# Kernel tuning notes

Hardware: AMD Instinct MI355X
Metric: run time of the kernel (lower is better)

The kernel has to match this reference:

```python
import jax, jax.numpy as jnp
import numpy as np

D_MODEL, D_INNER, D_STATE, D_CONV, DT_RANK = 4, 8, 16, 4, 1


def _build_perms(N, H, W):
    # center-out 2D spatial order
    yy, xx = np.meshgrid(np.arange(H), np.arange(W), indexing='ij')
    cy, cx = H // 2, W // 2
    d2 = (yy - cy) ** 2 + (xx - cx) ** 2
    sp = np.argsort(d2.reshape(-1), kind='stable')          # (H*W,)
    HW = H * W
    # scanA: for each frame t, full center-out spatial sweep
    scanA = (np.arange(N)[:, None] * HW + sp[None, :]).reshape(-1)
    # scanB: for each spatial pos (in center-out order), zig-zag over frames
    fwd = np.arange(N)
    bwd = fwd[::-1]
    tids = np.where((np.arange(HW) % 2 == 0)[:, None], fwd[None, :], bwd[None, :])  # (HW, N)
    scanB = (tids * HW + sp[:, None]).reshape(-1)
    perms = np.stack([scanA, scanB, scanA[::-1], scanB[::-1]], axis=0)  # (4, L)
    return jnp.asarray(perms)


def _dwconv1d(x_bcl, w, b, pad, groups):
    # x: (B, C, L), w: (C, 1, K) depthwise
    y = jax.lax.conv_general_dilated(x_bcl, w, (1,), [pad],
                                     feature_group_count=groups,
                                     dimension_numbers=('NCH', 'OIH', 'NCH'))
    return y + b[None, :, None]


def _forward(x, dwconv_w, dwconv_b, in_proj_w, conv1d_w, conv1d_b,
             x_proj_w, dt_proj_w, dt_proj_b, A_log, Dp, out_proj_w, ln_g, ln_b):
    B, N, H, W = x.shape
    L = N * H * W
    perms = _build_perms(N, H, W)                 # (4, L) int, static
    xf = x.reshape(B, L)
    seqs = xf[:, perms]                            # (B, 4, L) gather along 4 scans
    seqs = _dwconv1d(seqs, dwconv_w, dwconv_b, (1, 1), 4)
    u = jax.nn.silu(seqs.transpose(0, 2, 1))       # (B, L, 4)
    # ---- Mamba(d_model=4) ----
    xz = jnp.einsum('bld,ed->ble', u, in_proj_w)   # (B, L, 2*d_inner)
    xm, z = xz[..., :D_INNER], xz[..., D_INNER:]
    xc = _dwconv1d(xm.transpose(0, 2, 1), conv1d_w, conv1d_b, (D_CONV - 1, 0), D_INNER)
    xm = jax.nn.silu(xc.transpose(0, 2, 1))        # (B, L, 8) causal conv + SiLU
    x_dbl = jnp.einsum('bld,ed->ble', xm, x_proj_w)  # (B, L, dt_rank+2*d_state)
    dt = x_dbl[..., :DT_RANK]
    Bm = x_dbl[..., DT_RANK:DT_RANK + D_STATE]     # (B, L, 16)
    Cm = x_dbl[..., DT_RANK + D_STATE:]            # (B, L, 16)
    dt = jax.nn.softplus(jnp.einsum('blr,dr->bld', dt, dt_proj_w) + dt_proj_b)  # (B, L, 8)
    A = -jnp.exp(A_log)                            # (8, 16)
    dA = jnp.exp(dt[..., None] * A)                # (B, L, 8, 16)
    dBx = dt[..., None] * Bm[:, :, None, :] * xm[..., None]  # (B, L, 8, 16)

    def step(h, inp):
        dA_t, dBx_t, C_t = inp
        h = dA_t * h + dBx_t                       # (B, 8, 16)
        return h, jnp.einsum('bds,bs->bd', h, C_t)

    h0 = jnp.zeros((B, D_INNER, D_STATE), x.dtype)
    _, ys = jax.lax.scan(step, h0, (dA.transpose(1, 0, 2, 3),
                                    dBx.transpose(1, 0, 2, 3),
                                    Cm.transpose(1, 0, 2)))
    y = ys.transpose(1, 0, 2) + xm * Dp            # (B, L, 8)
    y = y * jax.nn.silu(z)
    out = jnp.einsum('bld,ed->ble', y, out_proj_w)  # (B, L, 4)
    # ---- LayerNorm(4) ----
    mu = out.mean(-1, keepdims=True)
    var = ((out - mu) ** 2).mean(-1, keepdims=True)
    out = (out - mu) * jax.lax.rsqrt(var + 1e-5) * ln_g + ln_b
    # rec[:, inv[i]] = out[:, :, i]  <=>  rec_i = out[:, perms[i], i]
    rec = jnp.take_along_axis(out, perms.T[None], axis=1)  # (B, L, 4)
    return rec.mean(-1).reshape(B, N, H, W)


def setup_inputs() -> dict:
    key = jax.random.key(0)
    ks = jax.random.split(key, 12)
    s = 0.1
    x = jax.random.normal(ks[0], (4, 6, 128, 128), jnp.float32)
    return {
        'x': x,
        'dwconv_w': jax.random.normal(ks[1], (4, 1, 3), jnp.float32) * s,
        'dwconv_b': jnp.zeros((4,), jnp.float32),
        'in_proj_w': jax.random.normal(ks[2], (2 * D_INNER, D_MODEL), jnp.float32) * s,
        'conv1d_w': jax.random.normal(ks[3], (D_INNER, 1, D_CONV), jnp.float32) * s,
        'conv1d_b': jnp.zeros((D_INNER,), jnp.float32),
        'x_proj_w': jax.random.normal(ks[4], (DT_RANK + 2 * D_STATE, D_INNER), jnp.float32) * s,
        'dt_proj_w': jax.random.normal(ks[5], (D_INNER, DT_RANK), jnp.float32) * s,
        'dt_proj_b': jnp.full((D_INNER,), -2.0, jnp.float32),
        'A_log': jnp.log(jnp.tile(jnp.arange(1, D_STATE + 1, dtype=jnp.float32), (D_INNER, 1))),
        'Dp': jnp.ones((D_INNER,), jnp.float32),
        'out_proj_w': jax.random.normal(ks[6], (D_MODEL, D_INNER), jnp.float32) * s,
        'ln_g': jnp.ones((4,), jnp.float32),
        'ln_b': jnp.zeros((4,), jnp.float32),
    }


def reference(x, dwconv_w, dwconv_b, in_proj_w, conv1d_w, conv1d_b,
              x_proj_w, dt_proj_w, dt_proj_b, A_log, Dp, out_proj_w, ln_g, ln_b):
    return _forward(x, dwconv_w, dwconv_b, in_proj_w, conv1d_w, conv1d_b,
                    x_proj_w, dt_proj_w, dt_proj_b, A_log, Dp, out_proj_w, ln_g, ln_b)
```

## Files before the change

kernel.cpp:

```cpp
#include <hip/hip_runtime.h>
#include <math.h>

#define HWSZ  16384
#define LTOT  98304
#define NB    4
#define TCH   96
#define NCH   1024
#define GCH   64
#define NGRP  16
#define SD    100

__device__ __forceinline__ float siluf(float x){
  return x * __builtin_amdgcn_rcpf(1.f + __expf(-x));
}
__device__ __forceinline__ float softplusf(float x){
  return fmaxf(x, 0.f) + __logf(1.f + __expf(-fabsf(x)));
}

__device__ __forceinline__ float red16(float x){
  int v;
  v = __float_as_int(x);
  x += __int_as_float(__builtin_amdgcn_update_dpp(0, v, 0xB1, 0xF, 0xF, true));
  v = __float_as_int(x);
  x += __int_as_float(__builtin_amdgcn_update_dpp(0, v, 0x4E, 0xF, 0xF, true));
  v = __float_as_int(x);
  x += __int_as_float(__builtin_amdgcn_update_dpp(0, v, 0x141, 0xF, 0xF, true));
  v = __float_as_int(x);
  x += __int_as_float(__builtin_amdgcn_update_dpp(0, v, 0x140, 0xF, 0xF, true));
  return x;
}

__device__ __forceinline__ int rho0(int i, const int* __restrict__ sp){
  int n = i >> 14; int r = i & (HWSZ - 1);
  return (n << 14) + sp[r];
}
__device__ __forceinline__ int rho1(int i, const int* __restrict__ sp){
  unsigned ui = (unsigned)i;
  unsigned r = ui / 6u; unsigned n = ui - r * 6u;
  unsigned t = (r & 1u) ? (5u - n) : n;
  return (int)((t << 14) + (unsigned)sp[r]);
}

__global__ __launch_bounds__(256) void k_rank(int* __restrict__ sp){
  __shared__ int hist[8193];
  __shared__ int part[256];
  const int tid = threadIdx.x;
  for (int v = tid; v < 8193; v += 256) hist[v] = 0;
  __syncthreads();
  for (int jj = tid; jj < HWSZ; jj += 256){
    int dy = (jj >> 7) - 64, dx = (jj & 127) - 64;
    atomicAdd(&hist[dy*dy + dx*dx], 1);
  }
  __syncthreads();
  const int base = tid * 33;
  {
    int sum = 0;
    for (int m = 0; m < 33; ++m){ int v = base + m; if (v < 8193) sum += hist[v]; }
    part[tid] = sum;
  }
  __syncthreads();
  if (tid == 0){
    int run = 0;
    for (int t = 0; t < 256; ++t){ int c = part[t]; part[t] = run; run += c; }
  }
  __syncthreads();
  {
    int run = part[tid];
    for (int m = 0; m < 33; ++m){
      int v = base + m;
      if (v < 8193){ int c = hist[v]; hist[v] = run; run += c; }
    }
  }
  __syncthreads();

  const int j = blockIdx.x * 256 + tid;
  const int y = j >> 7, x = j & 127;
  const int dy = y - 64, dx = x - 64;
  const int v = dy*dy + dx*dx;
  int cnt = hist[v];
  const int r = __float2int_rd(sqrtf((float)v));
  int yp0 = 64 - r; if (yp0 < 0) yp0 = 0;
  int yp1 = 64 + r + 1; if (yp1 > y) yp1 = y;
  for (int yp = yp0; yp < yp1; ++yp){
    int dyp = yp - 64;
    int tt = v - dyp*dyp;
    int rr = __float2int_rn(sqrtf((float)tt));
    if (rr * rr == tt){
      cnt += (rr <= 64) ? 1 : 0;
      cnt += (rr >= 1 && rr <= 63) ? 1 : 0;
    }
  }
  if (x > 64) cnt += 1;
  sp[cnt] = j;
}

__global__ __launch_bounds__(128, 4)
void k_scan(const float* __restrict__ X,
            const float* __restrict__ dww, const float* __restrict__ dwb,
            const float* __restrict__ ipw,
            const float* __restrict__ c1w, const float* __restrict__ c1b,
            const float* __restrict__ xpw,
            const float* __restrict__ dtpw, const float* __restrict__ dtpb,
            const float* __restrict__ Alog,
            const int* __restrict__ sp,
            float* __restrict__ chA, float* __restrict__ chB,
            float* __restrict__ y0g, float4* __restrict__ ug4)
{
  const int c = blockIdx.x, b = blockIdx.y;
  const int c0 = c * TCH;
  const int tid = threadIdx.x;
  const float* Xb = X + (size_t)b * LTOT;

  __shared__ __align__(16) float s_pre[(TCH + 3) * 9];
  __shared__ __align__(16) float s_dt[8 * SD];
  __shared__ __align__(16) float s_dxm[8 * SD];
  __shared__ __align__(16) float s_Bv[16 * SD];
  __shared__ __align__(16) float s_Cv[16 * SD];

  if (tid < TCH + 3){
    const int m = tid;
    const int i = c0 - 3 + m;
    if (i < 0){
      #pragma unroll
      for (int d = 0; d < 8; ++d) s_pre[m*9 + d] = 0.f;
    } else {
      const int i2 = LTOT - 1 - i;
      const bool okm = (i > 0), okp = (i < LTOT - 1);
      int q[12];
      q[0]  = okm ? rho0(i - 1, sp) : 0;
      q[1]  =       rho0(i,     sp);
      q[2]  = okp ? rho0(i + 1, sp) : 0;
      q[3]  = okm ? rho1(i - 1, sp) : 0;
      q[4]  =       rho1(i,     sp);
      q[5]  = okp ? rho1(i + 1, sp) : 0;
      q[6]  = okm ? rho0(i2 + 1, sp) : 0;
      q[7]  =       rho0(i2,     sp);
      q[8]  = okp ? rho0(i2 - 1, sp) : 0;
      q[9]  = okm ? rho1(i2 + 1, sp) : 0;
      q[10] =       rho1(i2,     sp);
      q[11] = okp ? rho1(i2 - 1, sp) : 0;
      float xv[12];
      #pragma unroll
      for (int t = 0; t < 12; ++t) xv[t] = Xb[q[t]];
      if (!okm){ xv[0] = 0.f; xv[3] = 0.f; xv[6] = 0.f; xv[9]  = 0.f; }
      if (!okp){ xv[2] = 0.f; xv[5] = 0.f; xv[8] = 0.f; xv[11] = 0.f; }
      float u[4];
      #pragma unroll
      for (int k = 0; k < 4; ++k){
        float acc = dwb[k];
        acc = fmaf(dww[k*3+0], xv[k*3+0], acc);
        acc = fmaf(dww[k*3+1], xv[k*3+1], acc);
        acc = fmaf(dww[k*3+2], xv[k*3+2], acc);
        u[k] = siluf(acc);
      }
      ug4[(size_t)b * LTOT + i] = make_float4(u[0], u[1], u[2], u[3]);
      #pragma unroll
      for (int d = 0; d < 8; ++d){
        float acc =      ipw[d*4+0] * u[0];
        acc = fmaf(ipw[d*4+1], u[1], acc);
        acc = fmaf(ipw[d*4+2], u[2], acc);
        acc = fmaf(ipw[d*4+3], u[3], acc);
        s_pre[m*9 + d] = acc;
      }
    }
  }
  __syncthreads();

  if (tid < TCH){
    const int t = tid;
    float xm[8];
    #pragma unroll
    for (int d = 0; d < 8; ++d){
      float acc = c1b[d];
      #pragma unroll
      for (int tau = 0; tau < 4; ++tau)
        acc = fmaf(c1w[d*4+tau], s_pre[(t+tau)*9 + d], acc);
      xm[d] = siluf(acc);
    }
    float dtr = xpw[0] * xm[0];
    #pragma unroll
    for (int d = 1; d < 8; ++d) dtr = fmaf(xpw[d], xm[d], dtr);
    #pragma unroll
    for (int s = 0; s < 16; ++s){
      float acc = xpw[(1+s)*8] * xm[0];
      #pragma unroll
      for (int d = 1; d < 8; ++d) acc = fmaf(xpw[(1+s)*8+d], xm[d], acc);
      s_Bv[s*SD + t] = acc;
      float acc2 = xpw[(17+s)*8] * xm[0];
      #pragma unroll
      for (int d = 1; d < 8; ++d) acc2 = fmaf(xpw[(17+s)*8+d], xm[d], acc2);
      s_Cv[s*SD + t] = acc2;
    }
    #pragma unroll
    for (int d = 0; d < 8; ++d){
      float dtv = softplusf(fmaf(dtpw[d], dtr, dtpb[d]));
      s_dt[d*SD + t]  = dtv;
      s_dxm[d*SD + t] = dtv * xm[d];
    }
  }
  __syncthreads();

  {
    const int d = tid >> 4, s = tid & 15;
    const float Ads = -__expf(Alog[tid]);
    float h = 0.f, sdt = 0.f;
    const float* pdt = s_dt + d*SD;
    const float* pdx = s_dxm + d*SD;
    const float* pB  = s_Bv + s*SD;
    const float* pC  = s_Cv + s*SD;
    float* yb = y0g + ((size_t)b * NCH + c) * 768 + d * 96;
    for (int t0 = 0; t0 < TCH; t0 += 4){
      const float4 dt4 = *reinterpret_cast<const float4*>(pdt + t0);
      const float4 dx4 = *reinterpret_cast<const float4*>(pdx + t0);
      const float4 B4  = *reinterpret_cast<const float4*>(pB + t0);
      const float4 C4  = *reinterpret_cast<const float4*>(pC + t0);
      sdt += dt4.x + dt4.y + dt4.z + dt4.w;
      float y0, y1, y2, y3;
      { float dA = __expf(dt4.x*Ads); h = fmaf(dA, h, dx4.x*B4.x); y0 = h*C4.x; }
      { float dA = __expf(dt4.y*Ads); h = fmaf(dA, h, dx4.y*B4.y); y1 = h*C4.y; }
      { float dA = __expf(dt4.z*Ads); h = fmaf(dA, h, dx4.z*B4.z); y2 = h*C4.z; }
      { float dA = __expf(dt4.w*Ads); h = fmaf(dA, h, dx4.w*B4.w); y3 = h*C4.w; }
      y0 = red16(y0); y1 = red16(y1); y2 = red16(y2); y3 = red16(y3);
      if (s == 0)
        *reinterpret_cast<float4*>(yb + t0) = make_float4(y0, y1, y2, y3);
    }
    const size_t base = ((size_t)b * NCH + c) * 128 + tid;
    chA[base] = __expf(Ads * sdt);
    chB[base] = h;
  }
}

__global__ __launch_bounds__(128) void k_comb1(const float* __restrict__ chA,
                                               const float* __restrict__ chB,
                                               float* __restrict__ hpre,
                                               float* __restrict__ apre,
                                               float* __restrict__ GA,
                                               float* __restrict__ GB){
  const int j = blockIdx.x;
  const int g = j >> 2, b = j & 3;
  const int idx = threadIdx.x;
  const size_t base = ((size_t)b * NCH + (size_t)g * GCH) * 128 + idx;
  float h = 0.f, a = 1.f;
  float A_[8], B_[8];
  #pragma unroll
  for (int m = 0; m < 8; ++m){ A_[m] = chA[base + (size_t)m*128]; B_[m] = chB[base + (size_t)m*128]; }
  for (int cc = 0; cc < GCH; cc += 8){
    float A2[8], B2[8];
    if (cc + 8 < GCH){
      #pragma unroll
      for (int m = 0; m < 8; ++m){ A2[m] = chA[base + (size_t)(cc+8+m)*128]; B2[m] = chB[base + (size_t)(cc+8+m)*128]; }
    } else {
      #pragma unroll
      for (int m = 0; m < 8; ++m){ A2[m] = 0.f; B2[m] = 0.f; }
    }
    #pragma unroll
    for (int m = 0; m < 8; ++m){
      hpre[base + (size_t)(cc+m)*128] = h;
      apre[base + (size_t)(cc+m)*128] = a;
      h = fmaf(A_[m], h, B_[m]);
      a *= A_[m];
    }
    #pragma unroll
    for (int m = 0; m < 8; ++m){ A_[m] = A2[m]; B_[m] = B2[m]; }
  }
  GA[(size_t)(g*4+b)*128 + idx] = a;
  GB[(size_t)(g*4+b)*128 + idx] = h;
}

#define NBL (NB * LTOT)
__global__ __launch_bounds__(128, 4)
void k_corr(const float4* __restrict__ ug4,
            const float* __restrict__ ipw,
            const float* __restrict__ c1w, const float* __restrict__ c1b,
            const float* __restrict__ xpw,
            const float* __restrict__ dtpw, const float* __restrict__ dtpb,
            const float* __restrict__ Alog, const float* __restrict__ Dp,
            const float* __restrict__ opw,
            const float* __restrict__ lng, const float* __restrict__ lnb,
            const float* __restrict__ hpre, const float* __restrict__ apre,
            const float* __restrict__ GA, const float* __restrict__ GB,
            const float* __restrict__ y0g,
            float* __restrict__ outbuf)
{
  const int c = blockIdx.x, b = blockIdx.y;
  const int c0 = c * TCH;
  const int tid = threadIdx.x;
  const size_t cb = (size_t)b * NCH + c;

  __shared__ __align__(16) float s_pre[(TCH + 3) * 9];
  __shared__ __align__(16) float s_sg[8 * 104];
  __shared__ __align__(16) float s_xm[8 * 96];
  __shared__ __align__(16) float s_Ct[96 * 20];
  __shared__ __align__(16) float s_zs[8 * 96];
  __shared__ __align__(16) float s_hA[256];
  float* s_yf = s_pre;

  {
    const int g = c >> 6;
    const float hp = hpre[cb * 128 + tid];
    const float ap = apre[cb * 128 + tid];
    float Hv = 0.f;
    for (int gp = 0; gp < g; ++gp){
      const float ga = GA[(size_t)gp*512 + (size_t)b*128 + tid];
      const float gb = GB[(size_t)gp*512 + (size_t)b*128 + tid];
      Hv = fmaf(ga, Hv, gb);
    }
    s_hA[tid]       = fmaf(ap, Hv, hp);
    s_hA[128 + tid] = -__expf(Alog[tid]);
  }

  if (tid < TCH + 3){
    const int m = tid;
    const int i = c0 - 3 + m;
    if (i < 0){
      #pragma unroll
      for (int d = 0; d < 8; ++d) s_pre[m*9 + d] = 0.f;
    } else {
      const float4 u4 = ug4[(size_t)b * LTOT + i];
      const float u[4] = {u4.x, u4.y, u4.z, u4.w};
      #pragma unroll
      for (int d = 0; d < 8; ++d){
        float acc =      ipw[d*4+0] * u[0];
        acc = fmaf(ipw[d*4+1], u[1], acc);
        acc = fmaf(ipw[d*4+2], u[2], acc);
        acc = fmaf(ipw[d*4+3], u[3], acc);
        s_pre[m*9 + d] = acc;
      }
      if (m >= 3){
        const int t0 = m - 3;
        #pragma unroll
        for (int d = 0; d < 8; ++d){
          float acc =      ipw[(8+d)*4+0] * u[0];
          acc = fmaf(ipw[(8+d)*4+1], u[1], acc);
          acc = fmaf(ipw[(8+d)*4+2], u[2], acc);
          acc = fmaf(ipw[(8+d)*4+3], u[3], acc);
          s_zs[d*96 + t0] = siluf(acc);
        }
      }
    }
  }
  __syncthreads();

  if (tid < TCH){
    const int t = tid;
    float xm[8];
    #pragma unroll
    for (int d = 0; d < 8; ++d){
      float acc = c1b[d];
      #pragma unroll
      for (int tau = 0; tau < 4; ++tau)
        acc = fmaf(c1w[d*4+tau], s_pre[(t+tau)*9 + d], acc);
      float v = siluf(acc);
      xm[d] = v;
      s_xm[d*96 + t] = v;
    }
    float dtr = xpw[0] * xm[0];
    #pragma unroll
    for (int d = 1; d < 8; ++d) dtr = fmaf(xpw[d], xm[d], dtr);
    float* pct = s_Ct + t*20;
    #pragma unroll
    for (int s = 0; s < 16; ++s){
      float acc2 = xpw[(17+s)*8] * xm[0];
      #pragma unroll
      for (int d = 1; d < 8; ++d) acc2 = fmaf(xpw[(17+s)*8+d], xm[d], acc2);
      pct[s] = acc2;
    }
    #pragma unroll
    for (int d = 0; d < 8; ++d)
      s_sg[d*104 + t] = softplusf(fmaf(dtpw[d], dtr, dtpb[d]));
  }
  __syncthreads();

  if (tid < 8){
    float* ps = s_sg + tid*104;
    float run = 0.f;
    for (int t0 = 0; t0 < TCH; t0 += 4){
      const float4 d4 = *reinterpret_cast<const float4*>(ps + t0);
      float r0 = run + d4.x, r1 = r0 + d4.y, r2 = r1 + d4.z, r3 = r2 + d4.w;
      *reinterpret_cast<float4*>(ps + t0) = make_float4(r0, r1, r2, r3);
      run = r3;
    }
  }
  __syncthreads();

  {
    const int d = tid >> 4, tsub = tid & 15;
    float w[16], A16[16];
    #pragma unroll
    for (int s = 0; s < 16; ++s){
      w[s]   = s_hA[d*16 + s];
      A16[s] = s_hA[128 + d*16 + s];
    }
    const float* py0 = y0g + cb * 768 + d * 96;
    for (int t = tsub; t < TCH; t += 16){
      const float sg = s_sg[d*104 + t];
      float acc = py0[t];
      const float* pc = s_Ct + t*20;
      #pragma unroll
      for (int s4 = 0; s4 < 16; s4 += 4){
        const float4 C4 = *reinterpret_cast<const float4*>(pc + s4);
        acc = fmaf(C4.x, __expf(A16[s4+0]*sg) * w[s4+0], acc);
        acc = fmaf(C4.y, __expf(A16[s4+1]*sg) * w[s4+1], acc);
        acc = fmaf(C4.z, __expf(A16[s4+2]*sg) * w[s4+2], acc);
        acc = fmaf(C4.w, __expf(A16[s4+3]*sg) * w[s4+3], acc);
      }
      s_yf[d*96 + t] = acc;
    }
  }
  __syncthreads();

  if (tid < TCH){
    const int t = tid;
    const int i = c0 + t;
    float y[8];
    #pragma unroll
    for (int d = 0; d < 8; ++d)
      y[d] = (s_yf[d*96 + t] + s_xm[d*96 + t] * Dp[d]) * s_zs[d*96 + t];
    float o[4];
    #pragma unroll
    for (int e = 0; e < 4; ++e){
      float acc = opw[e*8] * y[0];
      #pragma unroll
      for (int d = 1; d < 8; ++d) acc = fmaf(opw[e*8+d], y[d], acc);
      o[e] = acc;
    }
    const float mu = 0.25f * (o[0] + o[1] + o[2] + o[3]);
    const float v0 = o[0] - mu, v1 = o[1] - mu, v2 = o[2] - mu, v3 = o[3] - mu;
    const float inv = rsqrtf(0.25f * (v0*v0 + v1*v1 + v2*v2 + v3*v3) + 1e-5f);
    const size_t base = (size_t)b * LTOT + i;
    outbuf[0*NBL + base] = fmaf(v0 * inv, lng[0], lnb[0]);
    outbuf[1*NBL + base] = fmaf(v1 * inv, lng[1], lnb[1]);
    outbuf[2*NBL + base] = fmaf(v2 * inv, lng[2], lnb[2]);
    outbuf[3*NBL + base] = fmaf(v3 * inv, lng[3], lnb[3]);
  }
}

__global__ __launch_bounds__(256) void k_final(const float* __restrict__ outbuf,
                                               const int* __restrict__ sp,
                                               float* __restrict__ out){
  const int l = blockIdx.x * 256 + threadIdx.x;
  const int b = blockIdx.y;
  const int q0 = rho0(l, sp), q1 = rho1(l, sp);
  const int j  = LTOT - 1 - l;
  const int q2 = rho0(j, sp), q3 = rho1(j, sp);
  const size_t pb = (size_t)b * LTOT;
  out[pb + l] = 0.25f * (outbuf[0*NBL + pb + q0] + outbuf[1*NBL + pb + q1] +
                         outbuf[2*NBL + pb + q2] + outbuf[3*NBL + pb + q3]);
}

extern "C" void kernel_launch(void* const* d_in, const int* in_sizes, int n_in,
                              void* d_out, int out_size, void* d_ws, size_t ws_size,
                              hipStream_t stream) {
  const float* X    = (const float*)d_in[0];
  const float* dww  = (const float*)d_in[1];
  const float* dwb  = (const float*)d_in[2];
  const float* ipw  = (const float*)d_in[3];
  const float* c1w  = (const float*)d_in[4];
  const float* c1b  = (const float*)d_in[5];
  const float* xpw  = (const float*)d_in[6];
  const float* dtpw = (const float*)d_in[7];
  const float* dtpb = (const float*)d_in[8];
  const float* Alog = (const float*)d_in[9];
  const float* Dp   = (const float*)d_in[10];
  const float* opw  = (const float*)d_in[11];
  const float* lng  = (const float*)d_in[12];
  const float* lnb  = (const float*)d_in[13];
  float* out = (float*)d_out;

  int* wsI    = (int*)d_ws;
  int* sp     = wsI;
  float* chA  = (float*)(wsI + 16384);
  float* chB  = chA  + 524288;
  float* hpre = chB  + 524288;
  float* apre = hpre + 524288;
  float* GA   = apre + 524288;
  float* GB   = GA + 8192;
  float4* ug4 = (float4*)(GB + 8192);
  float* y0g  = (float*)(ug4) + (size_t)NB * LTOT * 4;
  float* outbuf = y0g + 3145728;

  k_rank<<<64, 256, 0, stream>>>(sp);
  k_scan<<<dim3(NCH, NB), 128, 0, stream>>>(X, dww, dwb, ipw, c1w, c1b, xpw,
      dtpw, dtpb, Alog, sp, chA, chB, y0g, ug4);
  k_comb1<<<64, 128, 0, stream>>>(chA, chB, hpre, apre, GA, GB);
  k_corr<<<dim3(NCH, NB), 128, 0, stream>>>(ug4, ipw, c1w, c1b, xpw,
      dtpw, dtpb, Alog, Dp, opw, lng, lnb, hpre, apre, GA, GB, y0g, outbuf);
  k_final<<<dim3(LTOT / 256, NB), 256, 0, stream>>>(outbuf, sp, out);
}
```

Before: 185.0 us.

## Store scan intermediates globally instead of recomputing them in correction pass

The scan kernel now writes the gate activations z, the conv outputs xm, the C projections and the per-chunk cumulative dt sums to global buffers. The correction kernel reads these back instead of recomputing the in-projection, causal conv, x-projection and softplus from the stored u values. This removes duplicated arithmetic and two block barriers from the correction pass. In exchange it adds much more global memory traffic, roughly 48 floats per position instead of 4.

```diff
diff --git a/kernel.cpp b/kernel.cpp
--- a/kernel.cpp
+++ b/kernel.cpp
@@ -9,6 +9,7 @@
 #define GCH   64
 #define NGRP  16
 #define SD    100
+#define NBL (NB * LTOT)
 
 __device__ __forceinline__ float siluf(float x){
   return x * __builtin_amdgcn_rcpf(1.f + __expf(-x));
@@ -104,7 +105,9 @@
             const float* __restrict__ Alog,
             const int* __restrict__ sp,
             float* __restrict__ chA, float* __restrict__ chB,
-            float* __restrict__ y0g, float4* __restrict__ ug4)
+            float* __restrict__ y0g, float* __restrict__ sgg,
+            float* __restrict__ xmg, float* __restrict__ zgg,
+            float* __restrict__ Cgg)
 {
   const int c = blockIdx.x, b = blockIdx.y;
   const int c0 = c * TCH;
@@ -153,7 +156,6 @@
         acc = fmaf(dww[k*3+2], xv[k*3+2], acc);
         u[k] = siluf(acc);
       }
-      ug4[(size_t)b * LTOT + i] = make_float4(u[0], u[1], u[2], u[3]);
       #pragma unroll
       for (int d = 0; d < 8; ++d){
         float acc =      ipw[d*4+0] * u[0];
@@ -162,6 +164,20 @@
         acc = fmaf(ipw[d*4+3], u[3], acc);
         s_pre[m*9 + d] = acc;
       }
+      if (m >= 3){
+        float zz[8];
+        #pragma unroll
+        for (int d = 0; d < 8; ++d){
+          float acc =      ipw[(8+d)*4+0] * u[0];
+          acc = fmaf(ipw[(8+d)*4+1], u[1], acc);
+          acc = fmaf(ipw[(8+d)*4+2], u[2], acc);
+          acc = fmaf(ipw[(8+d)*4+3], u[3], acc);
+          zz[d] = siluf(acc);
+        }
+        const size_t ib8 = ((size_t)b * LTOT + i) * 8;
+        *reinterpret_cast<float4*>(zgg + ib8)     = make_float4(zz[0], zz[1], zz[2], zz[3]);
+        *reinterpret_cast<float4*>(zgg + ib8 + 4) = make_float4(zz[4], zz[5], zz[6], zz[7]);
+      }
     }
   }
   __syncthreads();
@@ -177,9 +193,13 @@
         acc = fmaf(c1w[d*4+tau], s_pre[(t+tau)*9 + d], acc);
       xm[d] = siluf(acc);
     }
+    const size_t ib8 = ((size_t)b * LTOT + c0 + t) * 8;
+    *reinterpret_cast<float4*>(xmg + ib8)     = make_float4(xm[0], xm[1], xm[2], xm[3]);
+    *reinterpret_cast<float4*>(xmg + ib8 + 4) = make_float4(xm[4], xm[5], xm[6], xm[7]);
     float dtr = xpw[0] * xm[0];
     #pragma unroll
     for (int d = 1; d < 8; ++d) dtr = fmaf(xpw[d], xm[d], dtr);
+    float Cl[16];
     #pragma unroll
     for (int s = 0; s < 16; ++s){
       float acc = xpw[(1+s)*8] * xm[0];
@@ -190,7 +210,13 @@
       #pragma unroll
       for (int d = 1; d < 8; ++d) acc2 = fmaf(xpw[(17+s)*8+d], xm[d], acc2);
       s_Cv[s*SD + t] = acc2;
-    }
+      Cl[s] = acc2;
+    }
+    float* pcg = Cgg + ((size_t)b * LTOT + c0 + t) * 16;
+    *reinterpret_cast<float4*>(pcg)      = make_float4(Cl[0],  Cl[1],  Cl[2],  Cl[3]);
+    *reinterpret_cast<float4*>(pcg + 4)  = make_float4(Cl[4],  Cl[5],  Cl[6],  Cl[7]);
+    *reinterpret_cast<float4*>(pcg + 8)  = make_float4(Cl[8],  Cl[9],  Cl[10], Cl[11]);
+    *reinterpret_cast<float4*>(pcg + 12) = make_float4(Cl[12], Cl[13], Cl[14], Cl[15]);
     #pragma unroll
     for (int d = 0; d < 8; ++d){
       float dtv = softplusf(fmaf(dtpw[d], dtr, dtpb[d]));
@@ -203,18 +229,20 @@
   {
     const int d = tid >> 4, s = tid & 15;
     const float Ads = -__expf(Alog[tid]);
-    float h = 0.f, sdt = 0.f;
+    float h = 0.f, run = 0.f;
     const float* pdt = s_dt + d*SD;
     const float* pdx = s_dxm + d*SD;
     const float* pB  = s_Bv + s*SD;
     const float* pC  = s_Cv + s*SD;
     float* yb = y0g + ((size_t)b * NCH + c) * 768 + d * 96;
+    float* sb = sgg + ((size_t)b * NCH + c) * 768 + d * 96;
     for (int t0 = 0; t0 < TCH; t0 += 4){
       const float4 dt4 = *reinterpret_cast<const float4*>(pdt + t0);
       const float4 dx4 = *reinterpret_cast<const float4*>(pdx + t0);
       const float4 B4  = *reinterpret_cast<const float4*>(pB + t0);
       const float4 C4  = *reinterpret_cast<const float4*>(pC + t0);
-      sdt += dt4.x + dt4.y + dt4.z + dt4.w;
+      const float r0 = run + dt4.x, r1 = r0 + dt4.y, r2 = r1 + dt4.z, r3 = r2 + dt4.w;
+      run = r3;
       float y0, y1, y2, y3;
       { float dA = __expf(dt4.x*Ads); h = fmaf(dA, h, dx4.x*B4.x); y0 = h*C4.x; }
       { float dA = __expf(dt4.y*Ads); h = fmaf(dA, h, dx4.y*B4.y); y1 = h*C4.y; }
@@ -223,9 +251,11 @@
       y0 = red16(y0); y1 = red16(y1); y2 = red16(y2); y3 = red16(y3);
       if (s == 0)
         *reinterpret_cast<float4*>(yb + t0) = make_float4(y0, y1, y2, y3);
+      else if (s == 1)
+        *reinterpret_cast<float4*>(sb + t0) = make_float4(r0, r1, r2, r3);
     }
     const size_t base = ((size_t)b * NCH + c) * 128 + tid;
-    chA[base] = __expf(Ads * sdt);
+    chA[base] = __expf(Ads * run);
     chB[base] = h;
   }
 }
@@ -267,19 +297,15 @@
   GB[(size_t)(g*4+b)*128 + idx] = h;
 }
 
-#define NBL (NB * LTOT)
 __global__ __launch_bounds__(128, 4)
-void k_corr(const float4* __restrict__ ug4,
-            const float* __restrict__ ipw,
-            const float* __restrict__ c1w, const float* __restrict__ c1b,
-            const float* __restrict__ xpw,
-            const float* __restrict__ dtpw, const float* __restrict__ dtpb,
+void k_corr(const float* __restrict__ Cgg,
+            const float* __restrict__ xmg, const float* __restrict__ zgg,
+            const float* __restrict__ sgg, const float* __restrict__ y0g,
             const float* __restrict__ Alog, const float* __restrict__ Dp,
             const float* __restrict__ opw,
             const float* __restrict__ lng, const float* __restrict__ lnb,
             const float* __restrict__ hpre, const float* __restrict__ apre,
             const float* __restrict__ GA, const float* __restrict__ GB,
-            const float* __restrict__ y0g,
             float* __restrict__ outbuf)
 {
   const int c = blockIdx.x, b = blockIdx.y;
@@ -287,13 +313,8 @@
   const int tid = threadIdx.x;
   const size_t cb = (size_t)b * NCH + c;
 
-  __shared__ __align__(16) float s_pre[(TCH + 3) * 9];
-  __shared__ __align__(16) float s_sg[8 * 104];
-  __shared__ __align__(16) float s_xm[8 * 96];
-  __shared__ __align__(16) float s_Ct[96 * 20];
-  __shared__ __align__(16) float s_zs[8 * 96];
-  __shared__ __align__(16) float s_hA[256];
-  float* s_yf = s_pre;
+  __shared__ float s_hA[256];
+  __shared__ __align__(16) float s_yf[768];
 
   {
     const int g = c >> 6;
@@ -308,79 +329,6 @@
     s_hA[tid]       = fmaf(ap, Hv, hp);
     s_hA[128 + tid] = -__expf(Alog[tid]);
   }
-
-  if (tid < TCH + 3){
-    const int m = tid;
-    const int i = c0 - 3 + m;
-    if (i < 0){
-      #pragma unroll
-      for (int d = 0; d < 8; ++d) s_pre[m*9 + d] = 0.f;
-    } else {
-      const float4 u4 = ug4[(size_t)b * LTOT + i];
-      const float u[4] = {u4.x, u4.y, u4.z, u4.w};
-      #pragma unroll
-      for (int d = 0; d < 8; ++d){
-        float acc =      ipw[d*4+0] * u[0];
-        acc = fmaf(ipw[d*4+1], u[1], acc);
-        acc = fmaf(ipw[d*4+2], u[2], acc);
-        acc = fmaf(ipw[d*4+3], u[3], acc);
-        s_pre[m*9 + d] = acc;
-      }
-      if (m >= 3){
-        const int t0 = m - 3;
-        #pragma unroll
-        for (int d = 0; d < 8; ++d){
-          float acc =      ipw[(8+d)*4+0] * u[0];
-          acc = fmaf(ipw[(8+d)*4+1], u[1], acc);
-          acc = fmaf(ipw[(8+d)*4+2], u[2], acc);
-          acc = fmaf(ipw[(8+d)*4+3], u[3], acc);
-          s_zs[d*96 + t0] = siluf(acc);
-        }
-      }
-    }
-  }
-  __syncthreads();
-
-  if (tid < TCH){
-    const int t = tid;
-    float xm[8];
-    #pragma unroll
-    for (int d = 0; d < 8; ++d){
-      float acc = c1b[d];
-      #pragma unroll
-      for (int tau = 0; tau < 4; ++tau)
-        acc = fmaf(c1w[d*4+tau], s_pre[(t+tau)*9 + d], acc);
-      float v = siluf(acc);
-      xm[d] = v;
-      s_xm[d*96 + t] = v;
-    }
-    float dtr = xpw[0] * xm[0];
-    #pragma unroll
-    for (int d = 1; d < 8; ++d) dtr = fmaf(xpw[d], xm[d], dtr);
-    float* pct = s_Ct + t*20;
-    #pragma unroll
-    for (int s = 0; s < 16; ++s){
-      float acc2 = xpw[(17+s)*8] * xm[0];
-      #pragma unroll
-      for (int d = 1; d < 8; ++d) acc2 = fmaf(xpw[(17+s)*8+d], xm[d], acc2);
-      pct[s] = acc2;
-    }
-    #pragma unroll
-    for (int d = 0; d < 8; ++d)
-      s_sg[d*104 + t] = softplusf(fmaf(dtpw[d], dtr, dtpb[d]));
-  }
-  __syncthreads();
-
-  if (tid < 8){
-    float* ps = s_sg + tid*104;
-    float run = 0.f;
-    for (int t0 = 0; t0 < TCH; t0 += 4){
-      const float4 d4 = *reinterpret_cast<const float4*>(ps + t0);
-      float r0 = run + d4.x, r1 = r0 + d4.y, r2 = r1 + d4.z, r3 = r2 + d4.w;
-      *reinterpret_cast<float4*>(ps + t0) = make_float4(r0, r1, r2, r3);
-      run = r3;
-    }
-  }
   __syncthreads();
 
   {
@@ -391,11 +339,13 @@
       w[s]   = s_hA[d*16 + s];
       A16[s] = s_hA[128 + d*16 + s];
     }
+    const float* psg = sgg + cb * 768 + d * 96;
     const float* py0 = y0g + cb * 768 + d * 96;
+    const float* pC0 = Cgg + ((size_t)b * LTOT + c0) * 16;
     for (int t = tsub; t < TCH; t += 16){
-      const float sg = s_sg[d*104 + t];
+      const float sg = psg[t];
       float acc = py0[t];
-      const float* pc = s_Ct + t*20;
+      const float* pc = pC0 + t*16;
       #pragma unroll
       for (int s4 = 0; s4 < 16; s4 += 4){
         const float4 C4 = *reinterpret_cast<const float4*>(pc + s4);
@@ -412,10 +362,20 @@
   if (tid < TCH){
     const int t = tid;
     const int i = c0 + t;
+    const size_t ib8 = ((size_t)b * LTOT + i) * 8;
+    const float4 x0 = *reinterpret_cast<const float4*>(xmg + ib8);
+    const float4 x1 = *reinterpret_cast<const float4*>(xmg + ib8 + 4);
+    const float4 z0 = *reinterpret_cast<const float4*>(zgg + ib8);
+    const float4 z1 = *reinterpret_cast<const float4*>(zgg + ib8 + 4);
     float y[8];
-    #pragma unroll
-    for (int d = 0; d < 8; ++d)
-      y[d] = (s_yf[d*96 + t] + s_xm[d*96 + t] * Dp[d]) * s_zs[d*96 + t];
+    y[0] = fmaf(x0.x, Dp[0], s_yf[0*96 + t]) * z0.x;
+    y[1] = fmaf(x0.y, Dp[1], s_yf[1*96 + t]) * z0.y;
+    y[2] = fmaf(x0.z, Dp[2], s_yf[2*96 + t]) * z0.z;
+    y[3] = fmaf(x0.w, Dp[3], s_yf[3*96 + t]) * z0.w;
+    y[4] = fmaf(x1.x, Dp[4], s_yf[4*96 + t]) * z1.x;
+    y[5] = fmaf(x1.y, Dp[5], s_yf[5*96 + t]) * z1.y;
+    y[6] = fmaf(x1.z, Dp[6], s_yf[6*96 + t]) * z1.z;
+    y[7] = fmaf(x1.w, Dp[7], s_yf[7*96 + t]) * z1.w;
     float o[4];
     #pragma unroll
     for (int e = 0; e < 4; ++e){
@@ -475,15 +435,18 @@
   float* apre = hpre + 524288;
   float* GA   = apre + 524288;
   float* GB   = GA + 8192;
-  float4* ug4 = (float4*)(GB + 8192);
-  float* y0g  = (float*)(ug4) + (size_t)NB * LTOT * 4;
-  float* outbuf = y0g + 3145728;
+  float* y0g  = GB + 8192;
+  float* sgg  = y0g + 3145728;
+  float* xmg  = sgg + 3145728;
+  float* zgg  = xmg + 3145728;
+  float* Cgg  = zgg + 3145728;
+  float* outbuf = Cgg + 6291456;
 
   k_rank<<<64, 256, 0, stream>>>(sp);
   k_scan<<<dim3(NCH, NB), 128, 0, stream>>>(X, dww, dwb, ipw, c1w, c1b, xpw,
-      dtpw, dtpb, Alog, sp, chA, chB, y0g, ug4);
+      dtpw, dtpb, Alog, sp, chA, chB, y0g, sgg, xmg, zgg, Cgg);
   k_comb1<<<64, 128, 0, stream>>>(chA, chB, hpre, apre, GA, GB);
-  k_corr<<<dim3(NCH, NB), 128, 0, stream>>>(ug4, ipw, c1w, c1b, xpw,
-      dtpw, dtpb, Alog, Dp, opw, lng, lnb, hpre, apre, GA, GB, y0g, outbuf);
+  k_corr<<<dim3(NCH, NB), 128, 0, stream>>>(Cgg, xmg, zgg, sgg, y0g,
+      Alog, Dp, opw, lng, lnb, hpre, apre, GA, GB, outbuf);
   k_final<<<dim3(LTOT / 256, NB), 256, 0, stream>>>(outbuf, sp, out);
 }
```

Result: no change. 182.9 us (-1.1%).
